# Optimization experiments

Hardware: AMD Instinct MI355X
Metric: run time of the kernel (lower is better)

Reference implementation:

```python
import jax, jax.numpy as jnp
import numpy as np

N = 150000      # active voxels
C = 64          # head input channels
KK = 9          # 3x3 kernel offsets
H = W = 700     # BEV feature map
BN_EPS = 1e-5
HEADS = [("heatmap", 3), ("center", 2), ("center_z", 1), ("dim", 3), ("rot", 2)]


def _build_neighbor_table(seed=0):
    """Submanifold 3x3 neighbor indices for N active voxels on an HxW grid.
    Entry -1 means the neighbor site is inactive (contributes zero)."""
    rng = np.random.default_rng(seed)
    flat = rng.choice(H * W, size=N, replace=False)
    ys, xs = flat // W, flat % W
    lut = np.full(H * W, -1, np.int64)
    lut[flat] = np.arange(N)
    nbr = np.full((N, KK), -1, np.int64)
    k = 0
    for dy in (-1, 0, 1):
        for dx in (-1, 0, 1):
            ny, nx = ys + dy, xs + dx
            valid = (ny >= 0) & (ny < H) & (nx >= 0) & (nx < W)
            nf = np.where(valid, ny * W + nx, 0)
            nbr[:, k] = np.where(valid, lut[nf], -1)
            k += 1
    return nbr


def setup_inputs() -> dict:
    key = jax.random.key(0)
    ks = jax.random.split(key, 2 + 2 * len(HEADS))
    inp = {
        "features": jax.random.normal(ks[0], (N, C), jnp.float32),
        "nbr_idx": jnp.asarray(_build_neighbor_table(), jnp.int32),
        # one 3x3 subm conv per head, stacked: [n_heads, 9, C_in, C_out]
        "W3": jax.random.normal(ks[1], (len(HEADS), KK, C, C), jnp.float32) * 0.05,
        "gamma": jnp.ones((len(HEADS), C), jnp.float32),
        "beta": jnp.zeros((len(HEADS), C), jnp.float32),
    }
    for i, (name, oc) in enumerate(HEADS):
        inp[f"W1_{name}"] = jax.random.normal(ks[2 + i], (C, oc), jnp.float32) * 0.001
        if name == "heatmap":
            inp[f"b1_{name}"] = jnp.full((oc,), -float(np.log((1 - 0.01) / 0.01)), jnp.float32)
        else:
            inp[f"b1_{name}"] = jnp.zeros((oc,), jnp.float32)
    return inp


def _forward(features, nbr_idx, W3, gamma, beta, W1s, b1s):
    valid = nbr_idx >= 0                                  # [N, 9]
    idx = jnp.where(valid, nbr_idx, 0)
    # gather active-neighbor features; missing neighbors -> zero (subm conv)
    gathered = features[idx] * valid[..., None].astype(features.dtype)  # [N, 9, C]
    # all heads share the same input sparse tensor -> batched gather-GEMM
    h = jnp.einsum('nkc,hkco->hno', gathered, W3)         # [n_heads, N, C]
    # BatchNorm1d (training-mode batch stats, biased var) + ReLU
    mean = h.mean(axis=1, keepdims=True)
    var = ((h - mean) ** 2).mean(axis=1, keepdims=True)
    hn = (h - mean) * jax.lax.rsqrt(var + BN_EPS)
    hn = jax.nn.relu(hn * gamma[:, None, :] + beta[:, None, :])
    # per-head 1x1 subm conv == linear on active features
    return tuple(hn[i] @ W1s[i] + b1s[i] for i in range(len(HEADS)))


def reference(features, nbr_idx, W3, gamma, beta,
              W1_heatmap, b1_heatmap, W1_center, b1_center,
              W1_center_z, b1_center_z, W1_dim, b1_dim, W1_rot, b1_rot):
    W1s = [W1_heatmap, W1_center, W1_center_z, W1_dim, W1_rot]
    b1s = [b1_heatmap, b1_center, b1_center_z, b1_dim, b1_rot]
    return _forward(features, nbr_idx, W3, gamma, beta, W1s, b1s)
```

## Files before the change

kernel.cpp:

```cpp
#include <hip/hip_runtime.h>

#define NVOX 150000
#define BM 128
#define MTILES 1172
#define SROW 150016
#define NCOL 320

typedef __attribute__((ext_vector_type(8))) short bf16x8;
typedef __attribute__((ext_vector_type(4))) float f32x4;

__device__ __forceinline__ unsigned short f2bf(float f) {
    unsigned u = __builtin_bit_cast(unsigned, f);
    u += 0x7fffu + ((u >> 16) & 1u);
    return (unsigned short)(u >> 16);
}

__device__ __forceinline__ void gld16(const void* g, void* l) {
    __builtin_amdgcn_global_load_lds(
        (const __attribute__((address_space(1))) unsigned int*)g,
        (__attribute__((address_space(3))) unsigned int*)l, 16, 0, 0);
}

__global__ void prep_feat(const float* __restrict__ src, unsigned short* __restrict__ dst) {
    int i = blockIdx.x * 256 + threadIdx.x;
    if (i < NVOX * 8) {
        const float* s = src + (size_t)i * 8;
        float4 a = *(const float4*)s;
        float4 b = *(const float4*)(s + 4);
        union { bf16x8 v; unsigned short u[8]; } r;
        r.u[0] = f2bf(a.x); r.u[1] = f2bf(a.y); r.u[2] = f2bf(a.z); r.u[3] = f2bf(a.w);
        r.u[4] = f2bf(b.x); r.u[5] = f2bf(b.y); r.u[6] = f2bf(b.z); r.u[7] = f2bf(b.w);
        *(bf16x8*)(dst + (size_t)i * 8) = r.v;
    } else if (i < NVOX * 8 + 8) {
        bf16x8 z = {0, 0, 0, 0, 0, 0, 0, 0};
        *(bf16x8*)(dst + (size_t)i * 8) = z;
    }
}

__global__ void prep_w3(const float* __restrict__ w3, unsigned short* __restrict__ bt,
                        float* __restrict__ stats) {
    int i = blockIdx.x * 256 + threadIdx.x;
    int h = i / 36864;
    int rem = i - h * 36864;
    int kk = rem >> 12;
    int c = (rem >> 6) & 63;
    int o = rem & 63;
    bt[(size_t)(((h * 9 + kk) * 8) + (c >> 3)) * 512 + o * 8 + (c & 7)] = f2bf(w3[i]);
    if (i < 2 * NCOL) stats[i] = 0.f;
}

__global__ __launch_bounds__(256, 3)
void gemm_kernel(const unsigned short* __restrict__ featB,
                 const unsigned short* __restrict__ Bt2,
                 const int* __restrict__ nbr,
                 unsigned short* __restrict__ hbuf,
                 float* __restrict__ stats) {
    __shared__ __align__(16) char smem[53760];
    constexpr int IDX_OFF = 49152;
    constexpr int SRED_OFF = 32768;

    int bid = blockIdx.x;
    int r = bid & 7, q = bid >> 3;
    int ntile = q % 5;
    int mtile = (q / 5) * 8 + r;
    if (mtile >= MTILES) return;
    int m0 = mtile * BM;
    int n0 = ntile * 64;

    int tid = threadIdx.x;
    int w = tid >> 6, lane = tid & 63;
    int quad = lane >> 4, m16 = lane & 15;

    for (int lin = tid; lin < BM * 9; lin += 256) {
        int row = lin / 9, kkq = lin - row * 9;
        int v = -1;
        if (m0 + row < NVOX) v = nbr[(size_t)(m0 + row) * 9 + kkq];
        *(int*)(smem + IDX_OFF + (kkq * BM + row) * 4) = ((v < 0) ? NVOX : v) * 128;
    }
    __syncthreads();

    int off0r[9], off1r[9];
#pragma unroll
    for (int kk = 0; kk < 9; ++kk) {
        off0r[kk] = *(const int*)(smem + IDX_OFF + (kk * BM + lane) * 4);
        off1r[kk] = *(const int*)(smem + IDX_OFF + (kk * BM + 64 + lane) * 4);
    }

    f32x4 acc[4][2];
#pragma unroll
    for (int mt = 0; mt < 4; ++mt)
#pragma unroll
        for (int nt = 0; nt < 2; ++nt)
            acc[mt][nt] = (f32x4){0.f, 0.f, 0.f, 0.f};

    const char* fb = (const char*)featB;
    const char* bsrc = (const char*)Bt2 + (size_t)ntile * 73728;
    char* sAb[2] = {smem, smem + 16384};
    char* sBb[2] = {smem + 32768, smem + 40960};

    int mrow = (w >> 1) * 64;
    int ncol = (w & 1) * 32;
    int c16a = w * 2, c16b = w * 2 + 1;

    auto stage = [&](char* sA, char* sB, int kk, int off0, int off1) {
        gld16(fb + off0 + c16a * 16, sA + c16a * 2048);
        gld16(fb + off1 + c16a * 16, sA + c16a * 2048 + 1024);
        gld16(fb + off0 + c16b * 16, sA + c16b * 2048);
        gld16(fb + off1 + c16b * 16, sA + c16b * 2048 + 1024);
        gld16(bsrc + (kk * 8 + c16a) * 1024 + lane * 16, sB + c16a * 1024);
        gld16(bsrc + (kk * 8 + c16b) * 1024 + lane * 16, sB + c16b * 1024);
    };

    stage(sAb[0], sBb[0], 0, off0r[0], off1r[0]);
    __syncthreads();

#pragma unroll
    for (int kk = 0; kk < 9; ++kk) {
        const int cur = kk & 1;
        if (kk < 8)
            stage(sAb[cur ^ 1], sBb[cur ^ 1], kk + 1, off0r[kk + 1], off1r[kk + 1]);
        bf16x8 af[2][4], bfr[2][2];
#pragma unroll
        for (int ks = 0; ks < 2; ++ks) {
#pragma unroll
            for (int mt = 0; mt < 4; ++mt)
                af[ks][mt] = *(const bf16x8*)(sAb[cur] + (ks * 4 + quad) * 2048 +
                                              (mrow + mt * 16 + m16) * 16);
#pragma unroll
            for (int nt = 0; nt < 2; ++nt)
                bfr[ks][nt] = *(const bf16x8*)(sBb[cur] + (ks * 4 + quad) * 1024 +
                                               (ncol + nt * 16 + m16) * 16);
        }
#pragma unroll
        for (int ks = 0; ks < 2; ++ks)
#pragma unroll
            for (int mt = 0; mt < 4; ++mt)
#pragma unroll
                for (int nt = 0; nt < 2; ++nt)
                    acc[mt][nt] = __builtin_amdgcn_mfma_f32_16x16x32_bf16(
                        af[ks][mt], bfr[ks][nt], acc[mt][nt], 0, 0, 0);
        __syncthreads();
    }

#pragma unroll
    for (int mt = 0; mt < 4; ++mt) {
#pragma unroll
        for (int nt = 0; nt < 2; ++nt) {
            int col = ncol + nt * 16 + m16;
            int row = mrow + mt * 16 + quad * 4;
            f32x4 v = acc[mt][nt];
            unsigned lo = (unsigned)f2bf(v.x) | ((unsigned)f2bf(v.y) << 16);
            unsigned hi = (unsigned)f2bf(v.z) | ((unsigned)f2bf(v.w) << 16);
            uint2 pk; pk.x = lo; pk.y = hi;
            *(uint2*)(smem + col * 272 + row * 2) = pk;
        }
    }
    __syncthreads();
#pragma unroll
    for (int it = 0; it < 8; ++it) {
        int col = it * 8 + (tid >> 5);
        int l32 = tid & 31;
        uint2 v = *(const uint2*)(smem + col * 272 + l32 * 8);
        *(uint2*)(hbuf + (size_t)(n0 + col) * SROW + m0 + l32 * 4) = v;
    }

    float s[2], ss[2];
#pragma unroll
    for (int nt = 0; nt < 2; ++nt) {
        float a = 0.f, b = 0.f;
#pragma unroll
        for (int mt = 0; mt < 4; ++mt) {
            f32x4 v = acc[mt][nt];
            a += v.x + v.y + v.z + v.w;
            b += v.x * v.x + v.y * v.y + v.z * v.z + v.w * v.w;
        }
        s[nt] = a; ss[nt] = b;
        s[nt] += __shfl_xor(s[nt], 16); s[nt] += __shfl_xor(s[nt], 32);
        ss[nt] += __shfl_xor(ss[nt], 16); ss[nt] += __shfl_xor(ss[nt], 32);
    }
    if (quad == 0) {
#pragma unroll
        for (int nt = 0; nt < 2; ++nt) {
            float* p = (float*)(smem + SRED_OFF + ((w * 2 + nt) * 16 + m16) * 8);
            p[0] = s[nt]; p[1] = ss[nt];
        }
    }
    __syncthreads();
    if (tid < 64) {
        int col = tid;
        int half = col >> 5, nt = (col >> 4) & 1, mc = col & 15;
        const float* p0 = (const float*)(smem + SRED_OFF + ((half * 2 + nt) * 16 + mc) * 8);
        const float* p1 = (const float*)(smem + SRED_OFF + (((2 + half) * 2 + nt) * 16 + mc) * 8);
        atomicAdd(&stats[n0 + col], p0[0] + p1[0]);
        atomicAdd(&stats[NCOL + n0 + col], p0[1] + p1[1]);
    }
}

__global__ __launch_bounds__(256)
void head_kernel(const unsigned short* __restrict__ hbuf,
                 const float* __restrict__ stats,
                 const float* __restrict__ gamma, const float* __restrict__ beta,
                 const float* __restrict__ W1_0, const float* __restrict__ W1_1,
                 const float* __restrict__ W1_2, const float* __restrict__ W1_3,
                 const float* __restrict__ W1_4,
                 const float* __restrict__ b1_0, const float* __restrict__ b1_1,
                 const float* __restrict__ b1_2, const float* __restrict__ b1_3,
                 const float* __restrict__ b1_4,
                 float* __restrict__ out) {
    __shared__ float sScale[64], sShift[64], sW1[192], sB1[3];
    int h = blockIdx.y;
    const float* W1; const float* b1; int oc; size_t obase;
    if (h == 0)      { W1 = W1_0; b1 = b1_0; oc = 3; obase = 0; }
    else if (h == 1) { W1 = W1_1; b1 = b1_1; oc = 2; obase = 450000; }
    else if (h == 2) { W1 = W1_2; b1 = b1_2; oc = 1; obase = 750000; }
    else if (h == 3) { W1 = W1_3; b1 = b1_3; oc = 3; obase = 900000; }
    else             { W1 = W1_4; b1 = b1_4; oc = 2; obase = 1350000; }

    int tid = threadIdx.x;
    if (tid < 64) {
        int c = h * 64 + tid;
        float mean = stats[c] * (1.f / (float)NVOX);
        float var = stats[NCOL + c] * (1.f / (float)NVOX) - mean * mean;
        float inv = rsqrtf(var + 1e-5f);
        float sc = inv * gamma[c];
        sScale[tid] = sc;
        sShift[tid] = beta[c] - mean * sc;
    }
    for (int i = tid; i < 192; i += 256) {
        int cc = i / 3, jj = i - cc * 3;
        sW1[i] = (jj < oc) ? W1[cc * oc + jj] : 0.f;
    }
    if (tid == 0) {
        sB1[0] = b1[0];
        sB1[1] = (oc >= 2) ? b1[1] : 0.f;
        sB1[2] = (oc >= 3) ? b1[2] : 0.f;
    }
    __syncthreads();

    int n = (blockIdx.x * 256 + tid) * 4;
    if (n >= NVOX) return;
    const unsigned short* hp = hbuf + (size_t)(h * 64) * SROW + n;
    float x[4][3];
#pragma unroll
    for (int rr = 0; rr < 4; ++rr) { x[rr][0] = sB1[0]; x[rr][1] = sB1[1]; x[rr][2] = sB1[2]; }
#pragma unroll 8
    for (int cc = 0; cc < 64; ++cc) {
        uint2 raw = *(const uint2*)(hp + (size_t)cc * SROW);
        float sc = sScale[cc], sh = sShift[cc];
        float w0 = sW1[cc * 3 + 0], w1 = sW1[cc * 3 + 1], w2 = sW1[cc * 3 + 2];
        float v0 = __builtin_bit_cast(float, raw.x << 16);
        float v1 = __builtin_bit_cast(float, raw.x & 0xffff0000u);
        float v2 = __builtin_bit_cast(float, raw.y << 16);
        float v3 = __builtin_bit_cast(float, raw.y & 0xffff0000u);
        v0 = fmaxf(v0 * sc + sh, 0.f); v1 = fmaxf(v1 * sc + sh, 0.f);
        v2 = fmaxf(v2 * sc + sh, 0.f); v3 = fmaxf(v3 * sc + sh, 0.f);
        x[0][0] += v0 * w0; x[0][1] += v0 * w1; x[0][2] += v0 * w2;
        x[1][0] += v1 * w0; x[1][1] += v1 * w1; x[1][2] += v1 * w2;
        x[2][0] += v2 * w0; x[2][1] += v2 * w1; x[2][2] += v2 * w2;
        x[3][0] += v3 * w0; x[3][1] += v3 * w1; x[3][2] += v3 * w2;
    }
#pragma unroll
    for (int rr = 0; rr < 4; ++rr) {
        float* op = out + obase + (size_t)(n + rr) * oc;
        op[0] = x[rr][0];
        if (oc >= 2) op[1] = x[rr][1];
        if (oc >= 3) op[2] = x[rr][2];
    }
}

extern "C" void kernel_launch(void* const* d_in, const int* in_sizes, int n_in,
                              void* d_out, int out_size, void* d_ws, size_t ws_size,
                              hipStream_t stream) {
    const float* features = (const float*)d_in[0];
    const int* nbr        = (const int*)d_in[1];
    const float* w3       = (const float*)d_in[2];
    const float* gamma    = (const float*)d_in[3];
    const float* beta     = (const float*)d_in[4];
    const float* W1_0 = (const float*)d_in[5];  const float* b1_0 = (const float*)d_in[6];
    const float* W1_1 = (const float*)d_in[7];  const float* b1_1 = (const float*)d_in[8];
    const float* W1_2 = (const float*)d_in[9];  const float* b1_2 = (const float*)d_in[10];
    const float* W1_3 = (const float*)d_in[11]; const float* b1_3 = (const float*)d_in[12];
    const float* W1_4 = (const float*)d_in[13]; const float* b1_4 = (const float*)d_in[14];
    float* out = (float*)d_out;

    char* ws = (char*)d_ws;
    unsigned short* featB = (unsigned short*)ws;
    unsigned short* Bt2   = (unsigned short*)(ws + 19200128);
    float* stats          = (float*)(ws + 19568768);
    unsigned short* hbuf  = (unsigned short*)(ws + 19571328);

    prep_feat<<<(NVOX * 8 + 8 + 255) / 256, 256, 0, stream>>>(features, featB);
    prep_w3<<<184320 / 256, 256, 0, stream>>>(w3, Bt2, stats);
    gemm_kernel<<<8 * 5 * 147, 256, 0, stream>>>(featB, Bt2, nbr, hbuf, stats);
    head_kernel<<<dim3(147, 5), 256, 0, stream>>>(hbuf, stats, gamma, beta,
        W1_0, W1_1, W1_2, W1_3, W1_4, b1_0, b1_1, b1_2, b1_3, b1_4, out);
}
```

Measured before the change: 224.7 us.

## Load B fragments directly into registers and pipeline gather with manual waitcnt

Drops the LDS staging of the weight (B) tiles. Each wave now loads its B fragments from global memory straight into double-buffered registers, which shrinks shared memory and allows four blocks per CU instead of three. The per-offset neighbor indices are read from LDS inside the loop instead of being held in 18 registers. Synchronisation uses explicit s_waitcnt vmcnt, raw s_barrier and setprio around the MFMA section to overlap the next stage's gathers with compute. The risk is a fragile hand-counted vmcnt, and the redundant B global loads across waves rely on cache hits.

```diff
diff --git a/kernel.cpp b/kernel.cpp
--- a/kernel.cpp
+++ b/kernel.cpp
@@ -49,14 +49,14 @@
     if (i < 2 * NCOL) stats[i] = 0.f;
 }
 
-__global__ __launch_bounds__(256, 3)
+__global__ __launch_bounds__(256, 4)
 void gemm_kernel(const unsigned short* __restrict__ featB,
                  const unsigned short* __restrict__ Bt2,
                  const int* __restrict__ nbr,
                  unsigned short* __restrict__ hbuf,
                  float* __restrict__ stats) {
-    __shared__ __align__(16) char smem[53760];
-    constexpr int IDX_OFF = 49152;
+    __shared__ __align__(16) char smem[37376];
+    constexpr int IDX_OFF = 32768;
     constexpr int SRED_OFF = 32768;
 
     int bid = blockIdx.x;
@@ -79,13 +79,6 @@
     }
     __syncthreads();
 
-    int off0r[9], off1r[9];
-#pragma unroll
-    for (int kk = 0; kk < 9; ++kk) {
-        off0r[kk] = *(const int*)(smem + IDX_OFF + (kk * BM + lane) * 4);
-        off1r[kk] = *(const int*)(smem + IDX_OFF + (kk * BM + 64 + lane) * 4);
-    }
-
     f32x4 acc[4][2];
 #pragma unroll
     for (int mt = 0; mt < 4; ++mt)
@@ -96,50 +89,67 @@
     const char* fb = (const char*)featB;
     const char* bsrc = (const char*)Bt2 + (size_t)ntile * 73728;
     char* sAb[2] = {smem, smem + 16384};
-    char* sBb[2] = {smem + 32768, smem + 40960};
 
     int mrow = (w >> 1) * 64;
     int ncol = (w & 1) * 32;
     int c16a = w * 2, c16b = w * 2 + 1;
-
-    auto stage = [&](char* sA, char* sB, int kk, int off0, int off1) {
+    const char* bb = bsrc + quad * 1024 + (ncol + m16) * 16;
+
+    bf16x8 bfr[2][2][2];
+
+    auto stageA = [&](char* sA, int off0, int off1) {
         gld16(fb + off0 + c16a * 16, sA + c16a * 2048);
         gld16(fb + off1 + c16a * 16, sA + c16a * 2048 + 1024);
         gld16(fb + off0 + c16b * 16, sA + c16b * 2048);
         gld16(fb + off1 + c16b * 16, sA + c16b * 2048 + 1024);
-        gld16(bsrc + (kk * 8 + c16a) * 1024 + lane * 16, sB + c16a * 1024);
-        gld16(bsrc + (kk * 8 + c16b) * 1024 + lane * 16, sB + c16b * 1024);
     };
 
-    stage(sAb[0], sBb[0], 0, off0r[0], off1r[0]);
-    __syncthreads();
+    {
+        int o0 = *(const int*)(smem + IDX_OFF + lane * 4);
+        int o1 = *(const int*)(smem + IDX_OFF + (64 + lane) * 4);
+        bfr[0][0][0] = *(const bf16x8*)(bb);
+        bfr[0][0][1] = *(const bf16x8*)(bb + 256);
+        bfr[0][1][0] = *(const bf16x8*)(bb + 4096);
+        bfr[0][1][1] = *(const bf16x8*)(bb + 4352);
+        stageA(sAb[0], o0, o1);
+    }
 
 #pragma unroll
     for (int kk = 0; kk < 9; ++kk) {
-        const int cur = kk & 1;
-        if (kk < 8)
-            stage(sAb[cur ^ 1], sBb[cur ^ 1], kk + 1, off0r[kk + 1], off1r[kk + 1]);
-        bf16x8 af[2][4], bfr[2][2];
+        const int p = kk & 1;
+        if (kk < 8) {
+            int o0 = *(const int*)(smem + IDX_OFF + ((kk + 1) * BM + lane) * 4);
+            int o1 = *(const int*)(smem + IDX_OFF + ((kk + 1) * BM + 64 + lane) * 4);
+            const char* bk = bb + (size_t)(kk + 1) * 8192;
+            bfr[p ^ 1][0][0] = *(const bf16x8*)(bk);
+            bfr[p ^ 1][0][1] = *(const bf16x8*)(bk + 256);
+            bfr[p ^ 1][1][0] = *(const bf16x8*)(bk + 4096);
+            bfr[p ^ 1][1][1] = *(const bf16x8*)(bk + 4352);
+            stageA(sAb[p ^ 1], o0, o1);
+            asm volatile("s_waitcnt vmcnt(8)" ::: "memory");
+        } else {
+            asm volatile("s_waitcnt vmcnt(0)" ::: "memory");
+        }
+        asm volatile("s_barrier" ::: "memory");
+        __builtin_amdgcn_sched_barrier(0);
+        __builtin_amdgcn_s_setprio(1);
 #pragma unroll
         for (int ks = 0; ks < 2; ++ks) {
+            bf16x8 af[4];
 #pragma unroll
             for (int mt = 0; mt < 4; ++mt)
-                af[ks][mt] = *(const bf16x8*)(sAb[cur] + (ks * 4 + quad) * 2048 +
-                                              (mrow + mt * 16 + m16) * 16);
-#pragma unroll
-            for (int nt = 0; nt < 2; ++nt)
-                bfr[ks][nt] = *(const bf16x8*)(sBb[cur] + (ks * 4 + quad) * 1024 +
-                                               (ncol + nt * 16 + m16) * 16);
-        }
-#pragma unroll
-        for (int ks = 0; ks < 2; ++ks)
+                af[mt] = *(const bf16x8*)(sAb[p] + (ks * 4 + quad) * 2048 +
+                                          (mrow + mt * 16 + m16) * 16);
 #pragma unroll
             for (int mt = 0; mt < 4; ++mt)
 #pragma unroll
                 for (int nt = 0; nt < 2; ++nt)
                     acc[mt][nt] = __builtin_amdgcn_mfma_f32_16x16x32_bf16(
-                        af[ks][mt], bfr[ks][nt], acc[mt][nt], 0, 0, 0);
-        __syncthreads();
+                        af[mt], bfr[p][ks][nt], acc[mt][nt], 0, 0, 0);
+        }
+        __builtin_amdgcn_s_setprio(0);
+        __builtin_amdgcn_sched_barrier(0);
+        asm volatile("s_barrier" ::: "memory");
     }
 
 #pragma unroll
```

New measurement: 223.7 us. No clear change (-0.4%).
